# Optimization experiments

Hardware: AMD Instinct MI355X
Metric: run time of the kernel (lower is better)

Reference implementation:

```python
import jax, jax.numpy as jnp
import numpy as np

D = 256      # model dim
H = 4        # heads
L = 6        # layers (shared weights)
N = 32768    # neuron dim; per-head hidden = N//H = 8192
VOCAB = 256
B, T = 2, 2048
EPS = 1e-5


def _ln(x):
    # LayerNorm over last dim, no affine (matches nn.LayerNorm(D, elementwise_affine=False))
    m = jnp.mean(x, axis=-1, keepdims=True)
    v = jnp.mean((x - m) ** 2, axis=-1, keepdims=True)
    return (x - m) * jax.lax.rsqrt(v + EPS)


def _rope(x):
    # x: [B, H, T, d]
    d = x.shape[-1]
    t = x.shape[-2]
    inv_freq = 1.0 / (10000.0 ** (jnp.arange(0, d, 2, dtype=jnp.float32) / d))
    freqs = jnp.arange(t, dtype=jnp.float32)[:, None] * inv_freq[None, :]  # [T, d/2]
    emb = jnp.concatenate([freqs, freqs], axis=-1)                          # [T, d]
    x1, x2 = x[..., : d // 2], x[..., d // 2 :]
    x_rot = jnp.concatenate([-x2, x1], axis=-1)
    return x * jnp.cos(emb) + x_rot * jnp.sin(emb)


def _linear_attn(q, k, v):
    # q,k: [B,H,T,n]; v: [B,T,D]. Raw (unnormalized) scores, STRICTLY causal mask
    # (tril with diagonal=-1, i.e. token t attends to s < t only), no softmax.
    qr = _rope(q)
    kr = _rope(k)
    scores = jnp.einsum('bhtn,bhsn->bhts', qr, kr)  # [B,H,T,T]
    t_idx = jnp.arange(q.shape[-2])
    mask = t_idx[:, None] > t_idx[None, :]          # strict lower triangle
    scores = jnp.where(mask, scores, jnp.zeros((), scores.dtype))
    return jnp.einsum('bhts,bsd->bhtd', scores, v)  # [B,H,T,D]


def setup_inputs() -> dict:
    key = jax.random.key(0)
    ks = jax.random.split(key, 6)
    idx = jax.random.randint(ks[0], (B, T), 0, VOCAB, dtype=jnp.int64)
    std = 0.02
    wte = std * jax.random.normal(ks[1], (VOCAB, D), dtype=jnp.float32)
    encoder = std * jax.random.normal(ks[2], (N, D), dtype=jnp.float32)
    decoder_x = std * jax.random.normal(ks[3], (H, D, N // H), dtype=jnp.float32)
    decoder_y = std * jax.random.normal(ks[4], (H, D, N // H), dtype=jnp.float32)
    readout = std * jax.random.normal(ks[5], (D, VOCAB), dtype=jnp.float32)
    return {"idx": idx, "wte": wte, "encoder": encoder,
            "decoder_x": decoder_x, "decoder_y": decoder_y, "readout": readout}


def reference(idx, wte, encoder, decoder_x, decoder_y, readout):
    # Dropout is identity in eval mode.
    v_ast = _ln(wte[idx])  # [B,T,D]
    for _ in range(L):  # weights SHARED across layers
        x = jax.nn.relu(jnp.einsum('btd,hdn->bhtn', v_ast, decoder_x))  # [B,H,T,N/H]
        a_ast = _linear_attn(x, x, v_ast)                               # [B,H,T,D]
        y = jax.nn.relu(jnp.einsum('bhtd,hdn->bhtn', _ln(a_ast), decoder_y)) * x
        y_flat = jnp.transpose(y, (0, 2, 1, 3)).reshape(y.shape[0], y.shape[2], N)  # [B,T,N]
        v_ast = _ln(v_ast + _ln(y_flat @ encoder))
    return v_ast @ readout  # [B,T,VOCAB]
```

## Files before the change

kernel.cpp:

```cpp
#include <hip/hip_runtime.h>
#include <stdint.h>

typedef unsigned short u16;
typedef __bf16 bfv8 __attribute__((ext_vector_type(8)));
typedef float f32x4 __attribute__((ext_vector_type(4)));

#define BM 128
#define BN 128
#define BK 32

__device__ __forceinline__ float b2f(u16 u){ union{float f; unsigned int i;} x; x.i = ((unsigned int)u)<<16; return x.f; }
__device__ __forceinline__ u16 f2b(float f){ union{float f; unsigned int i;} x; x.f = f; unsigned int r = x.i + 0x7fffu + ((x.i>>16)&1u); return (u16)(r>>16); }

__device__ __forceinline__ void load16_lds(const void* g, void* l){
  __builtin_amdgcn_global_load_lds(
      (const __attribute__((address_space(1))) void*)g,
      (__attribute__((address_space(3))) void*)l, 16, 0, 0);
}

__device__ __forceinline__ void swz(int& bx, int& by, int& bz){
  int gx = gridDim.x, gy = gridDim.y;
  int nw = gx*gy*gridDim.z;
  int flat = blockIdx.x + gx*(blockIdx.y + gy*blockIdx.z);
  int q = nw >> 3, r = nw & 7, xcd = flat & 7, i = flat >> 3;
  int wg = (xcd < r ? xcd*(q+1) : r*(q+1) + (xcd-r)*q) + i;
  bx = wg % gx; int t = wg / gx; by = t % gy; bz = t / gy;
}

struct GP {
  const u16* A; const u16* Bt; const u16* A2; const u16* Bt2;
  const u16* ct; const u16* st;
  float* Cf; u16* Cb; u16* Y;
  int bh0, zs, zm;
};

template<int LDA, int LDB, bool PAIRB>
__device__ __forceinline__ void kloop(const u16* A, const u16* Bt, int m0, int n0,
                                      int kbeg, int kend, u16* As, u16* Bs,
                                      f32x4 (&acc)[4][4]){
  const int tid = threadIdx.x;
  const int lane = tid & 63;
  const int wid = tid >> 6;
  const int wm = wid >> 1, wn = wid & 1;
  const int srow = tid >> 2, sslot = tid & 3;
  for (int k0 = kbeg; k0 < kend; k0 += BK){
    #pragma unroll
    for (int q = 0; q < 2; ++q){
      int row = q*64 + srow;
      int ks = sslot ^ ((row >> 1) & 3);
      load16_lds(A + (long)(m0 + row)*LDA + (k0 + ks*8), As + q*2048 + wid*512);
    }
    #pragma unroll
    for (int q = 0; q < 2; ++q){
      int row = q*64 + srow;
      int ks = sslot ^ ((row >> 1) & 3);
      long brow;
      if (PAIRB){ int wnb = row >> 6, sub = (row >> 5) & 1, r5 = row & 31;
                  brow = n0 + wnb*32 + r5 + sub*4096; }
      else brow = n0 + row;
      load16_lds(Bt + brow*(long)LDB + (k0 + ks*8), Bs + q*2048 + wid*512);
    }
    __syncthreads();
    bfv8 af[4], bf[4];
    const int r16 = lane & 15, s4 = lane >> 4;
    #pragma unroll
    for (int i = 0; i < 4; ++i){
      int ar = wm*64 + i*16 + r16;
      af[i] = *(const bfv8*)(As + ar*BK + ((s4 ^ ((ar>>1)&3))*8));
      int br = wn*64 + i*16 + r16;
      bf[i] = *(const bfv8*)(Bs + br*BK + ((s4 ^ ((br>>1)&3))*8));
    }
    #pragma unroll
    for (int i = 0; i < 4; ++i)
      #pragma unroll
      for (int j = 0; j < 4; ++j)
        acc[i][j] = __builtin_amdgcn_mfma_f32_16x16x32_bf16(af[i], bf[j], acc[i][j], 0,0,0);
    __syncthreads();
  }
}

#define EPI_SETUP const int lane = threadIdx.x & 63, wid = threadIdx.x >> 6; \
  const int wm = wid >> 1, wn = wid & 1; const int r16 = lane & 15, s4 = lane >> 4;

__global__ __launch_bounds__(256) void g_rope(GP p){
  int bx, by, bz; swz(bx, by, bz);
  const int m0 = by*BM, n0 = bx*64, z = bz;
  const int bh = p.bh0 + z, b = bh >> 2, h = bh & 3;
  __shared__ u16 As[BM*BK], Bs[BN*BK];
  f32x4 acc[4][4] = {};
  kloop<256,256,true>(p.A + (long)b*524288, p.Bt + (long)h*2097152, m0, n0, 0, 256, As, Bs, acc);
  EPI_SETUP
  #pragma unroll
  for (int i = 0; i < 4; ++i)
    #pragma unroll
    for (int j = 0; j < 2; ++j){
      int cl = n0 + wn*32 + j*16 + r16;
      #pragma unroll
      for (int v = 0; v < 4; ++v){
        int row = m0 + wm*64 + i*16 + s4*4 + v;
        float x1 = fmaxf(acc[i][j][v], 0.f);
        float x2 = fmaxf(acc[i][j+2][v], 0.f);
        float c = b2f(p.ct[(long)row*4096 + cl]);
        float s = b2f(p.st[(long)row*4096 + cl]);
        p.Cb[(long)z*16777216 + (long)row*8192 + cl]        = f2b(x1*c - x2*s);
        p.Cb[(long)z*16777216 + (long)row*8192 + cl + 4096] = f2b(x2*c + x1*s);
      }
    }
}

__global__ __launch_bounds__(256) void g_qk(GP p){
  int bx, by, bz; swz(bx, by, bz);
  const int m0 = by*BM, n0 = bx*BN, z = bz;
  if (n0 >= m0 + BM) return;
  __shared__ u16 As[BM*BK], Bs[BN*BK];
  f32x4 acc[4][4] = {};
  const u16* A = p.A + (long)z*16777216;
  kloop<8192,8192,false>(A, A, m0, n0, 0, 8192, As, Bs, acc);
  EPI_SETUP
  #pragma unroll
  for (int i = 0; i < 4; ++i)
    #pragma unroll
    for (int j = 0; j < 4; ++j){
      int col = n0 + wn*64 + j*16 + r16;
      #pragma unroll
      for (int v = 0; v < 4; ++v){
        int row = m0 + wm*64 + i*16 + s4*4 + v;
        p.Cb[(long)z*4194304 + (long)row*2048 + col] = f2b(row > col ? acc[i][j][v] : 0.f);
      }
    }
}

__global__ __launch_bounds__(256) void g_pv(GP p){
  int bx, by, bz; swz(bx, by, bz);
  const int m0 = by*BM, n0 = bx*BN;
  const int head = bz >> p.zs, sl = bz & p.zm;
  const int b = (p.bh0 + head) >> 2;
  const int kc = 2048 >> p.zs;
  const int kbeg = sl*kc;
  const int kend = min(min(2048, m0 + BM), kbeg + kc);
  __shared__ u16 As[BM*BK], Bs[BN*BK];
  f32x4 acc[4][4] = {};
  kloop<2048,2048,false>(p.A + (long)head*4194304, p.Bt + (long)b*524288, m0, n0, kbeg, kend, As, Bs, acc);
  EPI_SETUP
  #pragma unroll
  for (int i = 0; i < 4; ++i)
    #pragma unroll
    for (int j = 0; j < 4; ++j){
      int col = n0 + wn*64 + j*16 + r16;
      #pragma unroll
      for (int v = 0; v < 4; ++v){
        int row = m0 + wm*64 + i*16 + s4*4 + v;
        p.Cf[(long)bz*524288 + (long)row*256 + col] = acc[i][j][v];
      }
    }
}

__global__ __launch_bounds__(256) void g_fuse(GP p){
  int bx, by, bz; swz(bx, by, bz);
  const int m0 = by*BM, n0 = bx*BN, z = bz;
  const int bh = p.bh0 + z, b = bh >> 2, h = bh & 3;
  __shared__ u16 As[BM*BK], Bs[BN*BK];
  f32x4 acc1[4][4] = {}, acc2[4][4] = {};
  kloop<256,256,false>(p.A  + (long)z*524288, p.Bt  + (long)h*2097152, m0, n0, 0, 256, As, Bs, acc1);
  kloop<256,256,false>(p.A2 + (long)b*524288, p.Bt2 + (long)h*2097152, m0, n0, 0, 256, As, Bs, acc2);
  EPI_SETUP
  #pragma unroll
  for (int i = 0; i < 4; ++i)
    #pragma unroll
    for (int j = 0; j < 4; ++j){
      int col = n0 + wn*64 + j*16 + r16;
      #pragma unroll
      for (int v = 0; v < 4; ++v){
        int row = m0 + wm*64 + i*16 + s4*4 + v;
        p.Y[(long)z*16777216 + (long)row*8192 + col] =
            f2b(fmaxf(acc1[i][j][v], 0.f) * fmaxf(acc2[i][j][v], 0.f));
      }
    }
}

__global__ __launch_bounds__(256) void g_enc(GP p){
  int bx, by, bz; swz(bx, by, bz);
  const int m0 = by*BM, n0 = bx*BN;
  const int head = bz >> p.zs, sp = bz & p.zm;
  const int h = (p.bh0 + head) & 3;
  const int kc = 8192 >> p.zs;
  const int kbeg = sp*kc, kend = kbeg + kc;
  __shared__ u16 As[BM*BK], Bs[BN*BK];
  f32x4 acc[4][4] = {};
  kloop<8192,32768,false>(p.A + (long)head*16777216, p.Bt + (long)h*8192, m0, n0, kbeg, kend, As, Bs, acc);
  EPI_SETUP
  #pragma unroll
  for (int i = 0; i < 4; ++i)
    #pragma unroll
    for (int j = 0; j < 4; ++j){
      int col = n0 + wn*64 + j*16 + r16;
      #pragma unroll
      for (int v = 0; v < 4; ++v){
        int row = m0 + wm*64 + i*16 + s4*4 + v;
        p.Cf[(long)bz*524288 + (long)row*256 + col] = acc[i][j][v];
      }
    }
}

__global__ __launch_bounds__(256) void g_out(GP p){
  int bx, by, bz; swz(bx, by, bz); (void)bz;
  const int m0 = by*BM, n0 = bx*BN;
  __shared__ u16 As[BM*BK], Bs[BN*BK];
  f32x4 acc[4][4] = {};
  kloop<256,256,false>(p.A, p.Bt, m0, n0, 0, 256, As, Bs, acc);
  EPI_SETUP
  #pragma unroll
  for (int i = 0; i < 4; ++i)
    #pragma unroll
    for (int j = 0; j < 4; ++j){
      int col = n0 + wn*64 + j*16 + r16;
      #pragma unroll
      for (int v = 0; v < 4; ++v){
        int row = m0 + wm*64 + i*16 + s4*4 + v;
        p.Cf[(long)row*256 + col] = acc[i][j][v];
      }
    }
}


__device__ __forceinline__ float wave_sum(float v){
  #pragma unroll
  for (int o = 32; o > 0; o >>= 1) v += __shfl_down(v, o, 64);
  return v;
}
__device__ __forceinline__ float block_sum(float v, float* sm){
  v = wave_sum(v);
  __syncthreads();
  if ((threadIdx.x & 63) == 0) sm[threadIdx.x >> 6] = v;
  __syncthreads();
  return sm[0] + sm[1] + sm[2] + sm[3];
}

__global__ __launch_bounds__(256) void k_embed(const int* idx, const float* wte,
                                               float* v, u16* vbf, u16* vbt){
  __shared__ float sm[4];
  __shared__ int is64_s;
  int row = blockIdx.x, d = threadIdx.x;
  int oddnz = (d < 64) ? (idx[2*d + 1] != 0) : 0;
  unsigned long long mb = __ballot(oddnz);
  if (threadIdx.x == 0) is64_s = (mb == 0ULL);
  __syncthreads();
  int tok = is64_s ? idx[2*row] : idx[row];
  float x = wte[tok*256 + d];
  float m = block_sum(x, sm) * (1.f/256.f);
  float dd = x - m;
  float var = block_sum(dd*dd, sm) * (1.f/256.f);
  float y = dd * rsqrtf(var + 1e-5f);
  v[(long)row*256 + d] = y;
  vbf[(long)row*256 + d] = f2b(y);
  int b = row >> 11, t = row & 2047;
  vbt[((long)(b*256 + d))*2048 + t] = f2b(y);
}

__global__ __launch_bounds__(256) void k_ln(const float* abuf, u16* out, int pv){
  __shared__ float sm[4];
  int row = blockIdx.x, d = threadIdx.x;
  int head = row >> 11, t = row & 2047;
  float x = 0.f;
  for (int s = 0; s < pv; ++s) x += abuf[((long)(head*pv + s) << 19) + (long)t*256 + d];
  float m = block_sum(x, sm) * (1.f/256.f);
  float dd = x - m;
  float var = block_sum(dd*dd, sm) * (1.f/256.f);
  out[(long)row*256 + d] = f2b(dd * rsqrtf(var + 1e-5f));
}

__global__ __launch_bounds__(256) void k_acc(const float* part, float* t1,
                                             int bh0, int gc, int ps){
  int t = blockIdx.x, d = threadIdx.x;
  long o = (long)t*256 + d;
  float s0 = 0.f, s1 = 0.f;
  for (int z = 0; z < gc; ++z){
    float v = 0.f;
    for (int sp = 0; sp < ps; ++sp) v += part[((long)(z*ps + sp) << 19) + o];
    if (((bh0 + z) >> 2) == 0) s0 += v; else s1 += v;
  }
  #pragma unroll
  for (int b = 0; b < 2; ++b){
    int lo = bh0 > 4*b ? bh0 : 4*b;
    int hi = (bh0 + gc) < (4*b + 4) ? (bh0 + gc) : (4*b + 4);
    if (lo < hi){
      float s = b == 0 ? s0 : s1;
      if (lo == 4*b) t1[((long)b << 19) + o] = s;
      else           t1[((long)b << 19) + o] += s;
    }
  }
}

__global__ __launch_bounds__(256) void k_finish(const float* t1, float* v, u16* vbf, u16* vbt){
  __shared__ float sm[4];
  int row = blockIdx.x; int d = threadIdx.x;
  int b = row >> 11, t = row & 2047;
  float s = t1[(long)row*256 + d];
  float m = block_sum(s, sm) * (1.f/256.f);
  float dd = s - m;
  float var = block_sum(dd*dd, sm) * (1.f/256.f);
  float u = dd * rsqrtf(var + 1e-5f);
  float wv = v[(long)row*256 + d] + u;
  float m2 = block_sum(wv, sm) * (1.f/256.f);
  float d2 = wv - m2;
  float v2 = block_sum(d2*d2, sm) * (1.f/256.f);
  float y = d2 * rsqrtf(v2 + 1e-5f);
  v[(long)row*256 + d] = y;
  vbf[(long)row*256 + d] = f2b(y);
  vbt[((long)(b*256 + d))*2048 + t] = f2b(y);
}

__global__ __launch_bounds__(256) void k_cossin(u16* ct, u16* st){
  int tid = blockIdx.x*256 + threadIdx.x;
  int t = tid >> 12, i = tid & 4095;
  float f = powf(10000.0f, -(float)i * (1.0f/4096.0f));
  float a = (float)t * f;
  float s, c; sincosf(a, &s, &c);
  ct[tid] = f2b(c); st[tid] = f2b(s);
}

__global__ void k_transpose(const float* in, u16* out, int R, int C, long in_z, long out_z){
  __shared__ float tile[32][33];
  const float* I = in + (long)blockIdx.z * in_z;
  u16* O = out + (long)blockIdx.z * out_z;
  int c0 = blockIdx.x*32, r0 = blockIdx.y*32;
  int tx = threadIdx.x, ty = threadIdx.y;
  #pragma unroll
  for (int k = 0; k < 4; ++k){ int r = ty + k*8; tile[r][tx] = I[(long)(r0+r)*C + c0+tx]; }
  __syncthreads();
  #pragma unroll
  for (int k = 0; k < 4; ++k){ int r = ty + k*8; O[(long)(c0+r)*R + r0+tx] = f2b(tile[tx][r]); }
}


extern "C" void kernel_launch(void* const* d_in, const int* in_sizes, int n_in,
                              void* d_out, int out_size, void* d_ws, size_t ws_size,
                              hipStream_t stream){
  const int*   idx = (const int*)d_in[0];
  const float* wte = (const float*)d_in[1];
  const float* enc = (const float*)d_in[2];
  const float* dx  = (const float*)d_in[3];
  const float* dy  = (const float*)d_in[4];
  const float* ro  = (const float*)d_in[5];
  float* out = (float*)d_out;
  (void)in_sizes; (void)n_in; (void)out_size;

  const size_t base_b = 96600064UL;
  struct Cfg { int gc, pvs, pss; };
  const Cfg lad[] = {{8,2,3},{4,2,3},{2,2,3},{2,1,2},{1,2,3},{1,1,2},{1,0,1},{1,0,0}};
  Cfg cfg = lad[7];
  for (int i = 0; i < 8; ++i){
    size_t ch = (size_t)lad[i].gc * (33554432UL + 8388608UL + 1048576UL
               + ((size_t)(1 << lad[i].pvs))*2097152UL
               + ((size_t)(1 << lad[i].pss))*2097152UL);
    if (base_b + ch <= ws_size){ cfg = lad[i]; break; }
  }
  const int gc = cfg.gc, pvs = cfg.pvs, pss = cfg.pss;
  const int pv = 1 << pvs, ps = 1 << pss;

  char* w = (char*)d_ws;
  size_t off = 0;
  auto alloc = [&](size_t b){ size_t r = off; off += (b + 255) & ~(size_t)255; return r; };
  float* v_ast = (float*)(w + alloc(4096UL*256*4));
  u16*   v_bf  = (u16*)  (w + alloc(4096UL*256*2));
  u16*   v_bt  = (u16*)  (w + alloc(2UL*256*2048*2));
  u16*   dxT   = (u16*)  (w + alloc(4UL*8192*256*2));
  u16*   dyT   = (u16*)  (w + alloc(4UL*8192*256*2));
  u16*   encT  = (u16*)  (w + alloc(256UL*32768*2));
  u16*   roT   = (u16*)  (w + alloc(256UL*256*2));
  u16*   ct    = (u16*)  (w + alloc(2048UL*4096*2));
  u16*   st    = (u16*)  (w + alloc(2048UL*4096*2));
  float* t1    = (float*)(w + alloc(2UL*2048*256*4));
  u16*   xbuf  = (u16*)  (w + alloc((size_t)gc*33554432));
  u16*   scb   = (u16*)  (w + alloc((size_t)gc*8388608));
  u16*   lnAb  = (u16*)  (w + alloc((size_t)gc*1048576));
  float* abuf  = (float*)(w + alloc((size_t)gc*pv*2097152UL));
  float* part  = (float*)(w + alloc((size_t)gc*ps*2097152UL));

  dim3 tb(32, 8);
  k_cossin<<<32768, 256, 0, stream>>>(ct, st);
  k_transpose<<<dim3(256, 8, 4),  tb, 0, stream>>>(dx,  dxT,  256,   8192, 256L*8192, 8192L*256);
  k_transpose<<<dim3(256, 8, 4),  tb, 0, stream>>>(dy,  dyT,  256,   8192, 256L*8192, 8192L*256);
  k_transpose<<<dim3(8, 1024, 1), tb, 0, stream>>>(enc, encT, 32768, 256,  0, 0);
  k_transpose<<<dim3(8, 8, 1),    tb, 0, stream>>>(ro,  roT,  256,   256,  0, 0);
  k_embed<<<4096, 256, 0, stream>>>(idx, wte, v_ast, v_bf, v_bt);

  for (int l = 0; l < 6; ++l){
    for (int bh0 = 0; bh0 < 8; bh0 += gc){
      { GP g{}; g.bh0=bh0; g.A=v_bf; g.Bt=dxT; g.ct=ct; g.st=st; g.Cb=xbuf;
        g_rope<<<dim3(64,16,gc), 256, 0, stream>>>(g); }
      { GP g{}; g.bh0=bh0; g.A=xbuf; g.Cb=scb;
        g_qk<<<dim3(16,16,gc), 256, 0, stream>>>(g); }
      { GP g{}; g.bh0=bh0; g.A=scb; g.Bt=v_bt; g.Cf=abuf; g.zs=pvs; g.zm=pv-1;
        g_pv<<<dim3(2,16,gc*pv), 256, 0, stream>>>(g); }
      k_ln<<<gc*2048, 256, 0, stream>>>(abuf, lnAb, pv);
      { GP g{}; g.bh0=bh0; g.A=lnAb; g.Bt=dyT; g.A2=v_bf; g.Bt2=dxT; g.Y=xbuf;
        g_fuse<<<dim3(64,16,gc), 256, 0, stream>>>(g); }
      { GP g{}; g.bh0=bh0; g.A=xbuf; g.Bt=encT; g.Cf=part; g.zs=pss; g.zm=ps-1;
        g_enc<<<dim3(2,16,gc*ps), 256, 0, stream>>>(g); }
      k_acc<<<2048, 256, 0, stream>>>(part, t1, bh0, gc, ps);
    }
    k_finish<<<4096, 256, 0, stream>>>(t1, v_ast, v_bf, v_bt);
  }
  { GP g{}; g.A=v_bf; g.Bt=roT; g.Cf=out;
    g_out<<<dim3(2,32,1), 256, 0, stream>>>(g); }
}
```

Baseline: 7.835 ms.

## Double-buffer LDS tiles in GEMM k-loop to overlap global loads with MFMA

New measurement: 7.998 ms. 2.1% more time.

```diff
diff --git a/kernel.cpp b/kernel.cpp
--- a/kernel.cpp
+++ b/kernel.cpp
@@ -36,19 +36,23 @@
 
 template<int LDA, int LDB, bool PAIRB>
 __device__ __forceinline__ void kloop(const u16* A, const u16* Bt, int m0, int n0,
-                                      int kbeg, int kend, u16* As, u16* Bs,
+                                      int kbeg, int kend,
+                                      u16 (&As)[2][4096], u16 (&Bs)[2][4096],
                                       f32x4 (&acc)[4][4]){
   const int tid = threadIdx.x;
   const int lane = tid & 63;
   const int wid = tid >> 6;
   const int wm = wid >> 1, wn = wid & 1;
   const int srow = tid >> 2, sslot = tid & 3;
-  for (int k0 = kbeg; k0 < kend; k0 += BK){
+  const int nt = (kend - kbeg) / BK;
+  if (nt <= 0) return;
+
+  auto stage = [&](int k0, int buf){
     #pragma unroll
     for (int q = 0; q < 2; ++q){
       int row = q*64 + srow;
       int ks = sslot ^ ((row >> 1) & 3);
-      load16_lds(A + (long)(m0 + row)*LDA + (k0 + ks*8), As + q*2048 + wid*512);
+      load16_lds(A + (long)(m0 + row)*LDA + (k0 + ks*8), &As[buf][q*2048 + wid*512]);
     }
     #pragma unroll
     for (int q = 0; q < 2; ++q){
@@ -58,25 +62,37 @@
       if (PAIRB){ int wnb = row >> 6, sub = (row >> 5) & 1, r5 = row & 31;
                   brow = n0 + wnb*32 + r5 + sub*4096; }
       else brow = n0 + row;
-      load16_lds(Bt + brow*(long)LDB + (k0 + ks*8), Bs + q*2048 + wid*512);
-    }
-    __syncthreads();
+      load16_lds(Bt + brow*(long)LDB + (k0 + ks*8), &Bs[buf][q*2048 + wid*512]);
+    }
+  };
+
+  stage(kbeg, 0);
+  int cur = 0;
+  for (int t = 0; t < nt; ++t){
+    int tn = (t+1 < nt) ? (t+1) : t;
+    stage(kbeg + tn*BK, cur^1);
+    asm volatile("s_waitcnt vmcnt(4)" ::: "memory");
+    __builtin_amdgcn_s_barrier();
     bfv8 af[4], bf[4];
     const int r16 = lane & 15, s4 = lane >> 4;
     #pragma unroll
     for (int i = 0; i < 4; ++i){
       int ar = wm*64 + i*16 + r16;
-      af[i] = *(const bfv8*)(As + ar*BK + ((s4 ^ ((ar>>1)&3))*8));
+      af[i] = *(const bfv8*)(&As[cur][ar*BK + ((s4 ^ ((ar>>1)&3))*8)]);
       int br = wn*64 + i*16 + r16;
-      bf[i] = *(const bfv8*)(Bs + br*BK + ((s4 ^ ((br>>1)&3))*8));
+      bf[i] = *(const bfv8*)(&Bs[cur][br*BK + ((s4 ^ ((br>>1)&3))*8)]);
     }
     #pragma unroll
     for (int i = 0; i < 4; ++i)
       #pragma unroll
       for (int j = 0; j < 4; ++j)
         acc[i][j] = __builtin_amdgcn_mfma_f32_16x16x32_bf16(af[i], bf[j], acc[i][j], 0,0,0);
-    __syncthreads();
+    asm volatile("s_waitcnt lgkmcnt(0)" ::: "memory");
+    __builtin_amdgcn_s_barrier();
+    cur ^= 1;
   }
+  asm volatile("s_waitcnt vmcnt(0)" ::: "memory");
+  __builtin_amdgcn_s_barrier();
 }
 
 #define EPI_SETUP const int lane = threadIdx.x & 63, wid = threadIdx.x >> 6; \
@@ -86,7 +102,7 @@
   int bx, by, bz; swz(bx, by, bz);
   const int m0 = by*BM, n0 = bx*64, z = bz;
   const int bh = p.bh0 + z, b = bh >> 2, h = bh & 3;
-  __shared__ u16 As[BM*BK], Bs[BN*BK];
+  __shared__ u16 As[2][4096], Bs[2][4096];
   f32x4 acc[4][4] = {};
   kloop<256,256,true>(p.A + (long)b*524288, p.Bt + (long)h*2097152, m0, n0, 0, 256, As, Bs, acc);
   EPI_SETUP
@@ -112,7 +128,7 @@
   int bx, by, bz; swz(bx, by, bz);
   const int m0 = by*BM, n0 = bx*BN, z = bz;
   if (n0 >= m0 + BM) return;
-  __shared__ u16 As[BM*BK], Bs[BN*BK];
+  __shared__ u16 As[2][4096], Bs[2][4096];
   f32x4 acc[4][4] = {};
   const u16* A = p.A + (long)z*16777216;
   kloop<8192,8192,false>(A, A, m0, n0, 0, 8192, As, Bs, acc);
@@ -138,7 +154,7 @@
   const int kc = 2048 >> p.zs;
   const int kbeg = sl*kc;
   const int kend = min(min(2048, m0 + BM), kbeg + kc);
-  __shared__ u16 As[BM*BK], Bs[BN*BK];
+  __shared__ u16 As[2][4096], Bs[2][4096];
   f32x4 acc[4][4] = {};
   kloop<2048,2048,false>(p.A + (long)head*4194304, p.Bt + (long)b*524288, m0, n0, kbeg, kend, As, Bs, acc);
   EPI_SETUP
@@ -159,7 +175,7 @@
   int bx, by, bz; swz(bx, by, bz);
   const int m0 = by*BM, n0 = bx*BN, z = bz;
   const int bh = p.bh0 + z, b = bh >> 2, h = bh & 3;
-  __shared__ u16 As[BM*BK], Bs[BN*BK];
+  __shared__ u16 As[2][4096], Bs[2][4096];
   f32x4 acc1[4][4] = {}, acc2[4][4] = {};
   kloop<256,256,false>(p.A  + (long)z*524288, p.Bt  + (long)h*2097152, m0, n0, 0, 256, As, Bs, acc1);
   kloop<256,256,false>(p.A2 + (long)b*524288, p.Bt2 + (long)h*2097152, m0, n0, 0, 256, As, Bs, acc2);
@@ -185,7 +201,7 @@
   const int h = (p.bh0 + head) & 3;
   const int kc = 8192 >> p.zs;
   const int kbeg = sp*kc, kend = kbeg + kc;
-  __shared__ u16 As[BM*BK], Bs[BN*BK];
+  __shared__ u16 As[2][4096], Bs[2][4096];
   f32x4 acc[4][4] = {};
   kloop<8192,32768,false>(p.A + (long)head*16777216, p.Bt + (long)h*8192, m0, n0, kbeg, kend, As, Bs, acc);
   EPI_SETUP
@@ -205,7 +221,7 @@
 __global__ __launch_bounds__(256) void g_out(GP p){
   int bx, by, bz; swz(bx, by, bz); (void)bz;
   const int m0 = by*BM, n0 = bx*BN;
-  __shared__ u16 As[BM*BK], Bs[BN*BK];
+  __shared__ u16 As[2][4096], Bs[2][4096];
   f32x4 acc[4][4] = {};
   kloop<256,256,false>(p.A, p.Bt, m0, n0, 0, 256, As, Bs, acc);
   EPI_SETUP
```
